# Performance work log

Measured on AMD Instinct MI355X. Metric: run time of the kernel, lower is better.

Reference implementation:

```python
import jax, jax.numpy as jnp
import numpy as np

EPS = 1e-5


def conv1x1(x, w, b=None):
    # x: [B,C,H,W], w: [O,C] (1x1 conv kernel squeezed)
    y = jnp.einsum('bchw,oc->bohw', x, w)
    if b is not None:
        y = y + b[None, :, None, None]
    return y


def bn_inf(x, g, b, m, v):
    scale = g / jnp.sqrt(v + EPS)
    return (x - m[None, :, None, None]) * scale[None, :, None, None] + b[None, :, None, None]


def setup_inputs() -> dict:
    B, C, H, W = 2, 256, 80, 80
    Ck, Cv, Co = 64, 128, 256
    key = jax.random.key(0)
    ks = jax.random.split(key, 16)
    d = {}
    d['x'] = jax.random.normal(ks[0], (B, C, H, W), dtype=jnp.float32)
    d['y'] = jax.random.normal(ks[1], (B, C, H, W), dtype=jnp.float32)
    s = 1.0 / np.sqrt(C)
    d['fk_w'] = jax.random.normal(ks[2], (Ck, C), dtype=jnp.float32) * s
    d['fk_g'] = jnp.ones((Ck,), jnp.float32)
    d['fk_b'] = jnp.zeros((Ck,), jnp.float32)
    d['fk_m'] = jax.random.normal(ks[3], (Ck,), dtype=jnp.float32) * 0.1
    d['fk_v'] = jax.random.uniform(ks[4], (Ck,), minval=0.5, maxval=1.5, dtype=jnp.float32)
    d['fq_w'] = jax.random.normal(ks[5], (Ck, C), dtype=jnp.float32) * s
    d['fq_g'] = jnp.ones((Ck,), jnp.float32)
    d['fq_b'] = jnp.zeros((Ck,), jnp.float32)
    d['fq_m'] = jax.random.normal(ks[6], (Ck,), dtype=jnp.float32) * 0.1
    d['fq_v'] = jax.random.uniform(ks[7], (Ck,), minval=0.5, maxval=1.5, dtype=jnp.float32)
    d['fv_w'] = jax.random.normal(ks[8], (Cv, C), dtype=jnp.float32) * s
    d['fv_b'] = jnp.zeros((Cv,), jnp.float32)
    d['W_w'] = jax.random.normal(ks[9], (Co, Cv), dtype=jnp.float32) * (1.0 / np.sqrt(Cv))
    d['W_b'] = jnp.zeros((Co,), jnp.float32)
    d['gamma'] = jnp.array([0.5], jnp.float32)
    return d


def reference(x, y, fk_w, fk_g, fk_b, fk_m, fk_v, fq_w, fq_g, fq_b, fq_m, fq_v, fv_w, fv_b, W_w, W_b, gamma):
    B, C, H, W = x.shape
    Ck = fk_w.shape[0]
    Cv = fv_w.shape[0]
    N = H * W
    # key from x, query/value from y (1x1 conv + BN projections)
    k = bn_inf(conv1x1(x, fk_w), fk_g, fk_b, fk_m, fk_v).reshape(B, Ck, N)          # [B,Ck,N]
    q = bn_inf(conv1x1(y, fq_w), fq_g, fq_b, fq_m, fq_v).reshape(B, Ck, N)          # [B,Ck,N]
    v = conv1x1(y, fv_w, fv_b).reshape(B, Cv, N)                                     # [B,Cv,N]
    sim = jnp.einsum('bkn,bkm->bnm', q, k) * (Ck ** -0.5)                            # [B,N,N]
    sim = jax.nn.softmax(sim, axis=-1)
    ctx = jnp.einsum('bnm,bvm->bvn', sim, v).reshape(B, Cv, H, W)                    # [B,Cv,H,W]
    ctx = conv1x1(ctx, W_w, W_b)                                                     # [B,Co,H,W]
    return gamma[0] * ctx + x
```

## Files before the change

### kernel.cpp

```cpp
#include <hip/hip_runtime.h>
#include <math.h>

#define NB   2
#define CIN  256
#define NN   6400
#define CKd  64
#define CVd  128
#define COd  256

using bf16   = __bf16;
using bf16x4 = __attribute__((ext_vector_type(4))) bf16;
using bf16x8 = __attribute__((ext_vector_type(8))) bf16;
using f32x4  = __attribute__((ext_vector_type(4))) float;

__device__ __forceinline__ void lds_cp16(const void* g, void* l) {
    __builtin_amdgcn_global_load_lds((const __attribute__((address_space(1))) void*)g,
                                     (__attribute__((address_space(3))) void*)l, 16, 0, 0);
}

__global__ void prep_kernel(const float* __restrict__ fk_w, const float* __restrict__ fk_g,
                            const float* __restrict__ fk_b, const float* __restrict__ fk_m,
                            const float* __restrict__ fk_v,
                            const float* __restrict__ fq_w, const float* __restrict__ fq_g,
                            const float* __restrict__ fq_b, const float* __restrict__ fq_m,
                            const float* __restrict__ fq_v,
                            const float* __restrict__ fv_w, const float* __restrict__ fv_b,
                            const float* __restrict__ W_w,  const float* __restrict__ W_b,
                            bf16* __restrict__ wkb, bf16* __restrict__ wqb,
                            bf16* __restrict__ wvb, bf16* __restrict__ wob,
                            float* __restrict__ bias)
{
    const int idx = blockIdx.x * 256 + threadIdx.x;
    if (idx < 16384) {
        const int co = idx >> 8;
        const float a = fk_g[co] * rsqrtf(fk_v[co] + 1e-5f);
        wkb[idx] = (bf16)(fk_w[idx] * a);
    } else if (idx < 32768) {
        const int i = idx - 16384, co = i >> 8;
        const float a = fq_g[co] * rsqrtf(fq_v[co] + 1e-5f) * 0.125f;
        wqb[i] = (bf16)(fq_w[i] * a);
    } else if (idx < 65536) {
        const int i = idx - 32768;
        wvb[i] = (bf16)fv_w[i];
    } else if (idx < 98304) {
        const int i = idx - 65536;
        wob[i] = (bf16)W_w[i];
    } else if (idx < 98816) {
        const int j = idx - 98304;
        if (j < 64)       { const float a = fk_g[j] * rsqrtf(fk_v[j] + 1e-5f); bias[j] = fk_b[j] - fk_m[j] * a; }
        else if (j < 128) { const int c = j - 64; const float a = fq_g[c] * rsqrtf(fq_v[c] + 1e-5f); bias[j] = (fq_b[c] - fq_m[c] * a) * 0.125f; }
        else if (j < 256) bias[j] = fv_b[j - 128];
        else              bias[j] = W_b[j - 256];
    }
}

__launch_bounds__(256)
__global__ void tcvt_kernel(const float* __restrict__ x, const float* __restrict__ y,
                            bf16* __restrict__ xT, bf16* __restrict__ yT)
{
    __shared__ __align__(16) bf16 t_lds[64][68];
    const int b = blockIdx.z & 1;
    const float* src = (blockIdx.z >> 1) ? y : x;
    bf16* dst = (blockIdx.z >> 1) ? yT : xT;
    const int n0 = blockIdx.x * 64, c0 = blockIdx.y * 64;
    const int tid = threadIdx.x;
    const int nl = (tid & 15) * 4;
#pragma unroll
    for (int p = 0; p < 4; ++p) {
        const int cl = (tid >> 4) + p * 16;
        const float4 v = *(const float4*)(src + (size_t)(b * CIN + c0 + cl) * NN + n0 + nl);
        t_lds[nl + 0][cl] = (bf16)v.x;
        t_lds[nl + 1][cl] = (bf16)v.y;
        t_lds[nl + 2][cl] = (bf16)v.z;
        t_lds[nl + 3][cl] = (bf16)v.w;
    }
    __syncthreads();
#pragma unroll
    for (int p = 0; p < 4; ++p) {
        const int u = tid + p * 256;
        const int n = u >> 4, c4 = (u & 15) * 4;
        const bf16x4 pk = *(const bf16x4*)&t_lds[n][c4];
        *(bf16x4*)(dst + ((size_t)b * NN + n0 + n) * CIN + c0 + c4) = pk;
    }
}

__launch_bounds__(256, 2)
__global__ void projkqv_kernel(const bf16* __restrict__ xT, const bf16* __restrict__ yT,
                               const bf16* __restrict__ wkb, const bf16* __restrict__ wqb,
                               const bf16* __restrict__ wvb, const float* __restrict__ bias,
                               bf16* __restrict__ kb, bf16* __restrict__ qb, bf16* __restrict__ vb)
{
    __shared__ __align__(16) bf16 sbuf[64 * 256];
    __shared__ __align__(16) bf16 wbuf[64 * 256];

    const int tid  = threadIdx.x;
    const int lane = tid & 63, wav = tid >> 6;
    const int l15  = lane & 15, quad = lane >> 4;
    const int b    = blockIdx.z, m = blockIdx.y;
    const int n0   = blockIdx.x * 64;

    const bf16* srcg = ((m == 0) ? xT : yT) + ((size_t)b * NN + n0) * CIN;
    const bf16* wg   = (m == 0) ? wkb : (m == 1) ? wqb : (wvb + (size_t)(m - 2) * 64 * CIN);

    const int r2  = lane >> 5;
    const int c32 = lane & 31;
#pragma unroll
    for (int i = 0; i < 8; ++i) {
        const int rg = wav * 16 + i * 2;
        const int r  = rg + r2;
        const int cs = c32 ^ (r & 7);
        lds_cp16(srcg + (size_t)r * 256 + cs * 8, &sbuf[rg * 256]);
        lds_cp16(wg   + (size_t)r * 256 + cs * 8, &wbuf[rg * 256]);
    }
    __syncthreads();

    const int key = l15 & 7;
    f32x4 acc[4];
#pragma unroll
    for (int j = 0; j < 4; ++j) acc[j] = (f32x4){0.f, 0.f, 0.f, 0.f};

    if (m < 2) {
        const int arow = wav * 16 + l15;
#pragma unroll
        for (int k4 = 0; k4 < 32; k4 += 4) {
            const bf16x8 af = *(const bf16x8*)&sbuf[arow * 256 + ((k4 + quad) ^ key) * 8];
#pragma unroll
            for (int nt = 0; nt < 4; ++nt) {
                const int brow = nt * 16 + l15;
                const bf16x8 bfw = *(const bf16x8*)&wbuf[brow * 256 + ((k4 + quad) ^ key) * 8];
                acc[nt] = __builtin_amdgcn_mfma_f32_16x16x32_bf16(af, bfw, acc[nt], 0, 0, 0);
            }
        }
        const float* bs = bias + m * 64;
        bf16* dst = (m == 0) ? kb : qb;
        const int nb = n0 + wav * 16;
#pragma unroll
        for (int nt = 0; nt < 4; ++nt) {
            const float bv = bs[nt * 16 + l15];
#pragma unroll
            for (int r = 0; r < 4; ++r) {
                const int n = nb + quad * 4 + r;
                dst[((size_t)b * NN + n) * CKd + nt * 16 + l15] = (bf16)(acc[nt][r] + bv);
            }
        }
    } else {
        const int arow = wav * 16 + l15;
#pragma unroll
        for (int k4 = 0; k4 < 32; k4 += 4) {
            const bf16x8 af = *(const bf16x8*)&wbuf[arow * 256 + ((k4 + quad) ^ key) * 8];
#pragma unroll
            for (int nt = 0; nt < 4; ++nt) {
                const int brow = nt * 16 + l15;
                const bf16x8 bfy = *(const bf16x8*)&sbuf[brow * 256 + ((k4 + quad) ^ key) * 8];
                acc[nt] = __builtin_amdgcn_mfma_f32_16x16x32_bf16(af, bfy, acc[nt], 0, 0, 0);
            }
        }
        const int cv0 = (m - 2) * 64 + wav * 16;
#pragma unroll
        for (int r = 0; r < 4; ++r) {
            const int cv = cv0 + quad * 4 + r;
            const float bv = bias[128 + cv];
#pragma unroll
            for (int nt = 0; nt < 4; ++nt)
                vb[((size_t)b * CVd + cv) * NN + n0 + nt * 16 + l15] = (bf16)(acc[nt][r] + bv);
        }
    }
}

__launch_bounds__(256, 3)
__global__ void attn_kernel(const bf16* __restrict__ qb, const bf16* __restrict__ kb,
                            const bf16* __restrict__ vb,
                            bf16* __restrict__ pO, float* __restrict__ pl,
                            int tpc, int kmask, int kbits)
{
    __shared__ __align__(16) bf16 kbuf[2][64 * 64];
    __shared__ __align__(16) bf16 vbuf[2][128 * 64];
    __shared__ __align__(16) bf16 p_lds[4][2][16][64];

    const int lane = threadIdx.x & 63;
    const int wav  = threadIdx.x >> 6;
    const int l15  = lane & 15;
    const int quad = lane >> 4;
    const int r8   = lane >> 3;
    const int c_src = (lane & 7) ^ r8;
    const int sw   = l15 & 7;
    const int pkey = (l15 & 7) << 1;

    const int id    = blockIdx.x;
    const int ks    = id & kmask;
    const int b     = (id >> kbits) & 1;
    const int qtile = id >> (kbits + 1);
    const int q0    = qtile * 128 + wav * 32;

    const bf16* qrow = qb + (size_t)b * NN * CKd;
    const bf16* krow = kb + (size_t)b * NN * CKd;
    const bf16* vrow = vb + (size_t)b * CVd * NN;

    bf16x8 qf[2][2];
#pragma unroll
    for (int qt = 0; qt < 2; ++qt)
#pragma unroll
        for (int s = 0; s < 2; ++s)
            qf[qt][s] = *(const bf16x8*)(qrow + (size_t)(q0 + qt * 16 + l15) * CKd + s * 32 + quad * 8);

    f32x4 acc[2][8];
#pragma unroll
    for (int qt = 0; qt < 2; ++qt)
#pragma unroll
        for (int cv = 0; cv < 8; ++cv) acc[qt][cv] = (f32x4){0.f, 0.f, 0.f, 0.f};
    float psum[2] = {0.f, 0.f};

    const int t0  = ks * tpc;
    const int rem = 100 - t0;
    const int nt  = (tpc < rem) ? tpc : rem;

    auto stage = [&](int t, int bi) {
        const int key0 = t * 64;
        lds_cp16(krow + (size_t)(key0 + wav * 8 + r8) * CKd + c_src * 8,
                 &kbuf[bi][(wav * 8) * 64]);
        lds_cp16(krow + (size_t)(key0 + (wav + 4) * 8 + r8) * CKd + c_src * 8,
                 &kbuf[bi][((wav + 4) * 8) * 64]);
#pragma unroll
        for (int g4 = 0; g4 < 4; ++g4) {
            const int g = wav * 4 + g4;
            lds_cp16(vrow + (size_t)(g * 8 + r8) * NN + key0 + c_src * 8,
                     &vbuf[bi][(g * 8) * 64]);
        }
    };

    stage(t0, 0);

    for (int t = 0; t < nt; ++t) {
        __syncthreads();
        if (t + 1 < nt) stage(t0 + t + 1, (t + 1) & 1);
        const bf16* kcur = &kbuf[t & 1][0];
        const bf16* vcur = &vbuf[t & 1][0];

        f32x4 s4[2][4];
#pragma unroll
        for (int kt = 0; kt < 4; ++kt) {
            const int rr = kt * 16 + l15;
            const bf16x8 kf0 = *(const bf16x8*)&kcur[rr * 64 + ((quad ^ sw) * 8)];
            const bf16x8 kf1 = *(const bf16x8*)&kcur[rr * 64 + (((4 + quad) ^ sw) * 8)];
#pragma unroll
            for (int qt = 0; qt < 2; ++qt) {
                f32x4 z = (f32x4){0.f, 0.f, 0.f, 0.f};
                z = __builtin_amdgcn_mfma_f32_16x16x32_bf16(kf0, qf[qt][0], z, 0, 0, 0);
                z = __builtin_amdgcn_mfma_f32_16x16x32_bf16(kf1, qf[qt][1], z, 0, 0, 0);
                s4[qt][kt] = z;
            }
        }

#pragma unroll
        for (int qt = 0; qt < 2; ++qt) {
            float ps = 0.f;
#pragma unroll
            for (int kt = 0; kt < 4; ++kt) {
                bf16x4 pk;
#pragma unroll
                for (int r = 0; r < 4; ++r) {
                    const float p = exp2f(fmaf(s4[qt][kt][r], 1.4426950408889634f, -11.541560327111707f));
                    ps += p;
                    pk[r] = (bf16)p;
                }
                *(bf16x4*)&p_lds[wav][qt][l15][((kt * 4 + quad) ^ pkey) * 4] = pk;
            }
            psum[qt] += ps;
        }

        bf16x8 pf[2][2];
#pragma unroll
        for (int qt = 0; qt < 2; ++qt)
#pragma unroll
            for (int sp = 0; sp < 2; ++sp)
                pf[qt][sp] = *(const bf16x8*)&p_lds[wav][qt][l15][((sp * 8 + quad * 2) ^ pkey) * 4];

#pragma unroll
        for (int sp = 0; sp < 2; ++sp)
#pragma unroll
            for (int cvt = 0; cvt < 8; ++cvt) {
                const int rr = cvt * 16 + l15;
                const bf16x8 vf = *(const bf16x8*)&vcur[rr * 64 + (((sp * 4 + quad) ^ sw) * 8)];
                acc[0][cvt] = __builtin_amdgcn_mfma_f32_16x16x32_bf16(vf, pf[0][sp], acc[0][cvt], 0, 0, 0);
                acc[1][cvt] = __builtin_amdgcn_mfma_f32_16x16x32_bf16(vf, pf[1][sp], acc[1][cvt], 0, 0, 0);
            }
    }

    __syncthreads();
    bf16* tbuf = &p_lds[wav][0][0][0];
    const size_t pb = (size_t)ks * NB + b;
#pragma unroll
    for (int qt = 0; qt < 2; ++qt) {
        psum[qt] += __shfl_xor(psum[qt], 16);
        psum[qt] += __shfl_xor(psum[qt], 32);
#pragma unroll
        for (int cvt = 0; cvt < 8; ++cvt) {
            bf16x4 pk;
#pragma unroll
            for (int r = 0; r < 4; ++r) pk[r] = (bf16)acc[qt][cvt][r];
            const int u = (cvt * 4 + quad) ^ ((l15 & 15) << 1);
            *(bf16x4*)&tbuf[l15 * 128 + u * 4] = pk;
        }
#pragma unroll
        for (int j = 0; j < 4; ++j) {
            const int row = j * 4 + (lane >> 4);
            const int g   = ((lane & 15) * 2) ^ ((row & 15) << 1);
            const bf16x8 vv = *(const bf16x8*)&tbuf[row * 128 + g * 4];
            *(bf16x8*)(pO + (pb * NN + q0 + qt * 16) * CVd + j * 512 + lane * 8) = vv;
        }
        if (quad == 0) pl[pb * NN + q0 + qt * 16 + l15] = psum[qt];
    }
}

__launch_bounds__(256, 2)
__global__ void outproj_kernel(const bf16* __restrict__ pO, const float* __restrict__ pl,
                               const bf16* __restrict__ wob, const float* __restrict__ bias,
                               const float* __restrict__ x, const float* __restrict__ gam,
                               float* __restrict__ out, int KS)
{
    __shared__ __align__(16) bf16 wbuf[256 * 128];
    __shared__ __align__(16) bf16 cbuf[32 * 128];
    __shared__ float Lrow[32];

    const int tid  = threadIdx.x;
    const int lane = tid & 63, wav = tid >> 6;
    const int l15  = lane & 15, quad = lane >> 4;
    const int b    = blockIdx.y;
    const int n0   = blockIdx.x * 32;

    {
        const int r4 = lane >> 4;
        const int c  = lane & 15;
#pragma unroll
        for (int i = 0; i < 16; ++i) {
            const int rg = wav * 64 + i * 4;
            const int r  = rg + r4;
            const int cs = c ^ (r & 7);
            lds_cp16(wob + (size_t)r * CVd + cs * 8, &wbuf[rg * 128]);
        }
    }

    const int tn = tid >> 3;
    const int tc = (tid & 7) * 16;
    float vacc[16];
#pragma unroll
    for (int i = 0; i < 16; ++i) vacc[i] = 0.f;
    for (int ksi = 0; ksi < KS; ++ksi) {
        const bf16* src = pO + ((size_t)(ksi * NB + b) * NN + n0 + tn) * CVd + tc;
#pragma unroll
        for (int j = 0; j < 2; ++j) {
            const bf16x8 v = *(const bf16x8*)(src + j * 8);
#pragma unroll
            for (int e = 0; e < 8; ++e) vacc[j * 8 + e] += (float)v[e];
        }
    }
    if (tid < 32) {
        float L = 0.f;
        for (int ksi = 0; ksi < KS; ++ksi)
            L += pl[(size_t)(ksi * NB + b) * NN + n0 + tid];
        Lrow[tid] = 1.0f / L;
    }
    __syncthreads();
    {
        const float rL = Lrow[tn];
#pragma unroll
        for (int j = 0; j < 2; ++j) {
            bf16x8 o;
#pragma unroll
            for (int e = 0; e < 8; ++e) o[e] = (bf16)(vacc[j * 8 + e] * rL);
            const int c = (tid & 7) * 2 + j;
            *(bf16x8*)&cbuf[tn * 128 + ((c ^ (tn & 7)) * 8)] = o;
        }
    }
    __syncthreads();

    f32x4 acc[4][2];
#pragma unroll
    for (int i = 0; i < 4; ++i)
#pragma unroll
        for (int j = 0; j < 2; ++j) acc[i][j] = (f32x4){0.f, 0.f, 0.f, 0.f};

#pragma unroll
    for (int kk = 0; kk < 4; ++kk) {
#pragma unroll
        for (int cot = 0; cot < 4; ++cot) {
            const int arow = wav * 64 + cot * 16 + l15;
            const bf16x8 af = *(const bf16x8*)&wbuf[arow * 128 + (((kk * 4 + quad) ^ (arow & 7)) * 8)];
#pragma unroll
            for (int nt = 0; nt < 2; ++nt) {
                const int brow = nt * 16 + l15;
                const bf16x8 bfc = *(const bf16x8*)&cbuf[brow * 128 + (((kk * 4 + quad) ^ (brow & 7)) * 8)];
                acc[cot][nt] = __builtin_amdgcn_mfma_f32_16x16x32_bf16(af, bfc, acc[cot][nt], 0, 0, 0);
            }
        }
    }

    const float gm = gam[0];
#pragma unroll
    for (int cot = 0; cot < 4; ++cot) {
#pragma unroll
        for (int r = 0; r < 4; ++r) {
            const int co = wav * 64 + cot * 16 + quad * 4 + r;
            const float bv = bias[256 + co];
#pragma unroll
            for (int nt = 0; nt < 2; ++nt) {
                const int n = n0 + nt * 16 + l15;
                const size_t a = ((size_t)b * COd + co) * NN + n;
                out[a] = gm * (acc[cot][nt][r] + bv) + x[a];
            }
        }
    }
}

extern "C" void kernel_launch(void* const* d_in, const int* in_sizes, int n_in,
                              void* d_out, int out_size, void* d_ws, size_t ws_size,
                              hipStream_t stream)
{
    const float* x     = (const float*)d_in[0];
    const float* y     = (const float*)d_in[1];
    const float* fk_w  = (const float*)d_in[2];
    const float* fk_g  = (const float*)d_in[3];
    const float* fk_b  = (const float*)d_in[4];
    const float* fk_m  = (const float*)d_in[5];
    const float* fk_v  = (const float*)d_in[6];
    const float* fq_w  = (const float*)d_in[7];
    const float* fq_g  = (const float*)d_in[8];
    const float* fq_b  = (const float*)d_in[9];
    const float* fq_m  = (const float*)d_in[10];
    const float* fq_v  = (const float*)d_in[11];
    const float* fv_w  = (const float*)d_in[12];
    const float* fv_b  = (const float*)d_in[13];
    const float* W_w   = (const float*)d_in[14];
    const float* W_b   = (const float*)d_in[15];
    const float* gamma = (const float*)d_in[16];
    float* out = (float*)d_out;

    char* ws = (char*)d_ws;
    size_t off = 0;
    auto carve = [&](size_t bytes) -> char* {
        char* p = ws + off;
        off = (off + bytes + 255) & ~(size_t)255;
        return p;
    };

    bf16*  kb   = (bf16*)carve((size_t)NB * NN * CKd * 2);
    bf16*  qbuf = (bf16*)carve((size_t)NB * NN * CKd * 2);
    bf16*  vb   = (bf16*)carve((size_t)NB * CVd * NN * 2);
    bf16*  wkb  = (bf16*)carve((size_t)CKd * CIN * 2);
    bf16*  wqb  = (bf16*)carve((size_t)CKd * CIN * 2);
    bf16*  wvb  = (bf16*)carve((size_t)CVd * CIN * 2);
    bf16*  wob  = (bf16*)carve((size_t)COd * CVd * 2);
    float* bias = (float*)carve(512 * 4);

    const size_t alias_start = off;
    bf16* xT = (bf16*)carve((size_t)NB * NN * CIN * 2);
    bf16* yT = (bf16*)carve((size_t)NB * NN * CIN * 2);

    const size_t region = ws_size - alias_start;
    const size_t per_ks = (size_t)NB * NN * CVd * 2 + (size_t)NB * NN * 4 + 512;
    int KS = 1, kbits = 0;
    {
        const int cand[4] = {8, 4, 2, 1};
        const int cbit[4] = {3, 2, 1, 0};
        for (int i = 0; i < 4; ++i)
            if ((size_t)cand[i] * per_ks <= region) { KS = cand[i]; kbits = cbit[i]; break; }
    }
    bf16*  pO = (bf16*)(ws + alias_start);
    float* pl = (float*)(ws + alias_start + (size_t)KS * NB * NN * CVd * 2);
    const int tpc = (100 + KS - 1) / KS;

    const dim3 blk(256);
    prep_kernel<<<386, blk, 0, stream>>>(fk_w, fk_g, fk_b, fk_m, fk_v,
                                         fq_w, fq_g, fq_b, fq_m, fq_v,
                                         fv_w, fv_b, W_w, W_b,
                                         wkb, wqb, wvb, wob, bias);
    tcvt_kernel<<<dim3(100, 4, 4), blk, 0, stream>>>(x, y, xT, yT);
    projkqv_kernel<<<dim3(100, 4, NB), blk, 0, stream>>>(xT, yT, wkb, wqb, wvb, bias, kb, qbuf, vb);
    attn_kernel<<<dim3(50 * NB * KS), blk, 0, stream>>>(qbuf, kb, vb, pO, pl, tpc, KS - 1, kbits);
    outproj_kernel<<<dim3(200, NB), blk, 0, stream>>>(pO, pl, wob, bias, x, gamma, out, KS);
}
```

Baseline: 189.9 us.

## Enlarge attention query tile per wave and fuse weight prep into transpose kernel

Each attention wave now handles 64 queries instead of 32, in two phases, so every K/V tile staged in LDS is reused across twice as many queries. The key-split factor can now be non-power-of-two (up to 10) to keep enough blocks in flight, and the grid is halved per split. The 1/sqrt(Ck) scale is folded together with log2(e) into the query weights, which removes an FMA in the softmax exponent. The separate weight-prep launch is merged into the transpose/convert kernel as an extra grid slice, saving one launch. The cost is more accumulator registers, so occupancy drops from 3 to 2 blocks per CU, and it adds integer division and modulo for the block index mapping.

```diff
diff --git a/kernel.cpp b/kernel.cpp
--- a/kernel.cpp
+++ b/kernel.cpp
@@ -18,47 +18,50 @@
                                      (__attribute__((address_space(3))) void*)l, 16, 0, 0);
 }
 
-__global__ void prep_kernel(const float* __restrict__ fk_w, const float* __restrict__ fk_g,
-                            const float* __restrict__ fk_b, const float* __restrict__ fk_m,
-                            const float* __restrict__ fk_v,
-                            const float* __restrict__ fq_w, const float* __restrict__ fq_g,
-                            const float* __restrict__ fq_b, const float* __restrict__ fq_m,
-                            const float* __restrict__ fq_v,
-                            const float* __restrict__ fv_w, const float* __restrict__ fv_b,
-                            const float* __restrict__ W_w,  const float* __restrict__ W_b,
-                            bf16* __restrict__ wkb, bf16* __restrict__ wqb,
-                            bf16* __restrict__ wvb, bf16* __restrict__ wob,
-                            float* __restrict__ bias)
-{
-    const int idx = blockIdx.x * 256 + threadIdx.x;
-    if (idx < 16384) {
-        const int co = idx >> 8;
-        const float a = fk_g[co] * rsqrtf(fk_v[co] + 1e-5f);
-        wkb[idx] = (bf16)(fk_w[idx] * a);
-    } else if (idx < 32768) {
-        const int i = idx - 16384, co = i >> 8;
-        const float a = fq_g[co] * rsqrtf(fq_v[co] + 1e-5f) * 0.125f;
-        wqb[i] = (bf16)(fq_w[i] * a);
-    } else if (idx < 65536) {
-        const int i = idx - 32768;
-        wvb[i] = (bf16)fv_w[i];
-    } else if (idx < 98304) {
-        const int i = idx - 65536;
-        wob[i] = (bf16)W_w[i];
-    } else if (idx < 98816) {
-        const int j = idx - 98304;
-        if (j < 64)       { const float a = fk_g[j] * rsqrtf(fk_v[j] + 1e-5f); bias[j] = fk_b[j] - fk_m[j] * a; }
-        else if (j < 128) { const int c = j - 64; const float a = fq_g[c] * rsqrtf(fq_v[c] + 1e-5f); bias[j] = (fq_b[c] - fq_m[c] * a) * 0.125f; }
-        else if (j < 256) bias[j] = fv_b[j - 128];
-        else              bias[j] = W_b[j - 256];
-    }
-}
-
 __launch_bounds__(256)
-__global__ void tcvt_kernel(const float* __restrict__ x, const float* __restrict__ y,
-                            bf16* __restrict__ xT, bf16* __restrict__ yT)
+__global__ void tcvt_prep_kernel(const float* __restrict__ x, const float* __restrict__ y,
+                                 bf16* __restrict__ xT, bf16* __restrict__ yT,
+                                 const float* __restrict__ fk_w, const float* __restrict__ fk_g,
+                                 const float* __restrict__ fk_b, const float* __restrict__ fk_m,
+                                 const float* __restrict__ fk_v,
+                                 const float* __restrict__ fq_w, const float* __restrict__ fq_g,
+                                 const float* __restrict__ fq_b, const float* __restrict__ fq_m,
+                                 const float* __restrict__ fq_v,
+                                 const float* __restrict__ fv_w, const float* __restrict__ fv_b,
+                                 const float* __restrict__ W_w,  const float* __restrict__ W_b,
+                                 bf16* __restrict__ wkb, bf16* __restrict__ wqb,
+                                 bf16* __restrict__ wvb, bf16* __restrict__ wob,
+                                 float* __restrict__ bias)
 {
     __shared__ __align__(16) bf16 t_lds[64][68];
+
+    if (blockIdx.z == 4) {
+        const int idx = (blockIdx.y * 100 + blockIdx.x) * 256 + threadIdx.x;
+        const float QS = 0.18033688011112042f;
+        if (idx < 16384) {
+            const int co = idx >> 8;
+            const float a = fk_g[co] * rsqrtf(fk_v[co] + 1e-5f);
+            wkb[idx] = (bf16)(fk_w[idx] * a);
+        } else if (idx < 32768) {
+            const int i = idx - 16384, co = i >> 8;
+            const float a = fq_g[co] * rsqrtf(fq_v[co] + 1e-5f) * QS;
+            wqb[i] = (bf16)(fq_w[i] * a);
+        } else if (idx < 65536) {
+            const int i = idx - 32768;
+            wvb[i] = (bf16)fv_w[i];
+        } else if (idx < 98304) {
+            const int i = idx - 65536;
+            wob[i] = (bf16)W_w[i];
+        } else if (idx < 98816) {
+            const int j = idx - 98304;
+            if (j < 64)       { const float a = fk_g[j] * rsqrtf(fk_v[j] + 1e-5f); bias[j] = fk_b[j] - fk_m[j] * a; }
+            else if (j < 128) { const int c = j - 64; const float a = fq_g[c] * rsqrtf(fq_v[c] + 1e-5f); bias[j] = (fq_b[c] - fq_m[c] * a) * QS; }
+            else if (j < 256) bias[j] = fv_b[j - 128];
+            else              bias[j] = W_b[j - 256];
+        }
+        return;
+    }
+
     const int b = blockIdx.z & 1;
     const float* src = (blockIdx.z >> 1) ? y : x;
     bf16* dst = (blockIdx.z >> 1) ? yT : xT;
@@ -167,11 +170,10 @@
     }
 }
 
-__launch_bounds__(256, 3)
+__launch_bounds__(256, 2)
 __global__ void attn_kernel(const bf16* __restrict__ qb, const bf16* __restrict__ kb,
                             const bf16* __restrict__ vb,
-                            bf16* __restrict__ pO, float* __restrict__ pl,
-                            int tpc, int kmask, int kbits)
+                            bf16* __restrict__ pO, float* __restrict__ pl, int KS)
 {
     __shared__ __align__(16) bf16 kbuf[2][64 * 64];
     __shared__ __align__(16) bf16 vbuf[2][128 * 64];
@@ -187,32 +189,32 @@
     const int pkey = (l15 & 7) << 1;
 
     const int id    = blockIdx.x;
-    const int ks    = id & kmask;
-    const int b     = (id >> kbits) & 1;
-    const int qtile = id >> (kbits + 1);
-    const int q0    = qtile * 128 + wav * 32;
+    const int ks    = id % KS;
+    const int rst   = id / KS;
+    const int b     = rst & 1;
+    const int qtile = rst >> 1;
+    const int q0    = qtile * 256 + wav * 64;
 
     const bf16* qrow = qb + (size_t)b * NN * CKd;
     const bf16* krow = kb + (size_t)b * NN * CKd;
     const bf16* vrow = vb + (size_t)b * CVd * NN;
 
-    bf16x8 qf[2][2];
-#pragma unroll
-    for (int qt = 0; qt < 2; ++qt)
+    bf16x8 qf[4][2];
+#pragma unroll
+    for (int qt = 0; qt < 4; ++qt)
 #pragma unroll
         for (int s = 0; s < 2; ++s)
             qf[qt][s] = *(const bf16x8*)(qrow + (size_t)(q0 + qt * 16 + l15) * CKd + s * 32 + quad * 8);
 
-    f32x4 acc[2][8];
-#pragma unroll
-    for (int qt = 0; qt < 2; ++qt)
+    f32x4 acc[4][8];
+#pragma unroll
+    for (int qt = 0; qt < 4; ++qt)
 #pragma unroll
         for (int cv = 0; cv < 8; ++cv) acc[qt][cv] = (f32x4){0.f, 0.f, 0.f, 0.f};
-    float psum[2] = {0.f, 0.f};
-
-    const int t0  = ks * tpc;
-    const int rem = 100 - t0;
-    const int nt  = (tpc < rem) ? tpc : rem;
+    float psum[4] = {0.f, 0.f, 0.f, 0.f};
+
+    const int t0 = (100 * ks) / KS;
+    const int nt = (100 * (ks + 1)) / KS - t0;
 
     auto stage = [&](int t, int bi) {
         const int key0 = t * 64;
@@ -236,61 +238,61 @@
         const bf16* kcur = &kbuf[t & 1][0];
         const bf16* vcur = &vbuf[t & 1][0];
 
-        f32x4 s4[2][4];
-#pragma unroll
-        for (int kt = 0; kt < 4; ++kt) {
-            const int rr = kt * 16 + l15;
-            const bf16x8 kf0 = *(const bf16x8*)&kcur[rr * 64 + ((quad ^ sw) * 8)];
-            const bf16x8 kf1 = *(const bf16x8*)&kcur[rr * 64 + (((4 + quad) ^ sw) * 8)];
-#pragma unroll
-            for (int qt = 0; qt < 2; ++qt) {
-                f32x4 z = (f32x4){0.f, 0.f, 0.f, 0.f};
-                z = __builtin_amdgcn_mfma_f32_16x16x32_bf16(kf0, qf[qt][0], z, 0, 0, 0);
-                z = __builtin_amdgcn_mfma_f32_16x16x32_bf16(kf1, qf[qt][1], z, 0, 0, 0);
-                s4[qt][kt] = z;
-            }
-        }
-
-#pragma unroll
-        for (int qt = 0; qt < 2; ++qt) {
-            float ps = 0.f;
+#pragma unroll
+        for (int ph = 0; ph < 2; ++ph) {
+            f32x4 s4[2][4];
 #pragma unroll
             for (int kt = 0; kt < 4; ++kt) {
-                bf16x4 pk;
-#pragma unroll
-                for (int r = 0; r < 4; ++r) {
-                    const float p = exp2f(fmaf(s4[qt][kt][r], 1.4426950408889634f, -11.541560327111707f));
-                    ps += p;
-                    pk[r] = (bf16)p;
+                const int rr = kt * 16 + l15;
+                const bf16x8 kf0 = *(const bf16x8*)&kcur[rr * 64 + ((quad ^ sw) * 8)];
+                const bf16x8 kf1 = *(const bf16x8*)&kcur[rr * 64 + (((4 + quad) ^ sw) * 8)];
+#pragma unroll
+                for (int qtl = 0; qtl < 2; ++qtl) {
+                    const int qt = ph * 2 + qtl;
+                    f32x4 z = (f32x4){0.f, 0.f, 0.f, 0.f};
+                    z = __builtin_amdgcn_mfma_f32_16x16x32_bf16(kf0, qf[qt][0], z, 0, 0, 0);
+                    z = __builtin_amdgcn_mfma_f32_16x16x32_bf16(kf1, qf[qt][1], z, 0, 0, 0);
+                    s4[qtl][kt] = z;
                 }
-                *(bf16x4*)&p_lds[wav][qt][l15][((kt * 4 + quad) ^ pkey) * 4] = pk;
-            }
-            psum[qt] += ps;
-        }
-
-        bf16x8 pf[2][2];
-#pragma unroll
-        for (int qt = 0; qt < 2; ++qt)
-#pragma unroll
-            for (int sp = 0; sp < 2; ++sp)
-                pf[qt][sp] = *(const bf16x8*)&p_lds[wav][qt][l15][((sp * 8 + quad * 2) ^ pkey) * 4];
-
-#pragma unroll
-        for (int sp = 0; sp < 2; ++sp)
-#pragma unroll
-            for (int cvt = 0; cvt < 8; ++cvt) {
-                const int rr = cvt * 16 + l15;
-                const bf16x8 vf = *(const bf16x8*)&vcur[rr * 64 + (((sp * 4 + quad) ^ sw) * 8)];
-                acc[0][cvt] = __builtin_amdgcn_mfma_f32_16x16x32_bf16(vf, pf[0][sp], acc[0][cvt], 0, 0, 0);
-                acc[1][cvt] = __builtin_amdgcn_mfma_f32_16x16x32_bf16(vf, pf[1][sp], acc[1][cvt], 0, 0, 0);
-            }
+            }
+
+#pragma unroll
+            for (int qtl = 0; qtl < 2; ++qtl) {
+                float ps = 0.f;
+#pragma unroll
+                for (int kt = 0; kt < 4; ++kt) {
+                    bf16x4 pk;
+#pragma unroll
+                    for (int r = 0; r < 4; ++r) {
+                        const float p = exp2f(s4[qtl][kt][r] - 11.541560327111707f);
+                        ps += p;
+                        pk[r] = (bf16)p;
+                    }
+                    *(bf16x4*)&p_lds[wav][qtl][l15][((kt * 4 + quad) ^ pkey) * 4] = pk;
+                }
+                psum[ph * 2 + qtl] += ps;
+            }
+
+#pragma unroll
+            for (int sp = 0; sp < 2; ++sp) {
+                const bf16x8 pf0 = *(const bf16x8*)&p_lds[wav][0][l15][((sp * 8 + quad * 2) ^ pkey) * 4];
+                const bf16x8 pf1 = *(const bf16x8*)&p_lds[wav][1][l15][((sp * 8 + quad * 2) ^ pkey) * 4];
+#pragma unroll
+                for (int cvt = 0; cvt < 8; ++cvt) {
+                    const int rr = cvt * 16 + l15;
+                    const bf16x8 vf = *(const bf16x8*)&vcur[rr * 64 + (((sp * 4 + quad) ^ sw) * 8)];
+                    acc[ph * 2 + 0][cvt] = __builtin_amdgcn_mfma_f32_16x16x32_bf16(vf, pf0, acc[ph * 2 + 0][cvt], 0, 0, 0);
+                    acc[ph * 2 + 1][cvt] = __builtin_amdgcn_mfma_f32_16x16x32_bf16(vf, pf1, acc[ph * 2 + 1][cvt], 0, 0, 0);
+                }
+            }
+        }
     }
 
     __syncthreads();
     bf16* tbuf = &p_lds[wav][0][0][0];
     const size_t pb = (size_t)ks * NB + b;
 #pragma unroll
-    for (int qt = 0; qt < 2; ++qt) {
+    for (int qt = 0; qt < 4; ++qt) {
         psum[qt] += __shfl_xor(psum[qt], 16);
         psum[qt] += __shfl_xor(psum[qt], 32);
 #pragma unroll
@@ -298,7 +300,7 @@
             bf16x4 pk;
 #pragma unroll
             for (int r = 0; r < 4; ++r) pk[r] = (bf16)acc[qt][cvt][r];
-            const int u = (cvt * 4 + quad) ^ ((l15 & 15) << 1);
+            const int u = (cvt * 4 + quad) ^ (l15 << 1);
             *(bf16x4*)&tbuf[l15 * 128 + u * 4] = pk;
         }
 #pragma unroll
@@ -458,24 +460,22 @@
 
     const size_t region = ws_size - alias_start;
     const size_t per_ks = (size_t)NB * NN * CVd * 2 + (size_t)NB * NN * 4 + 512;
-    int KS = 1, kbits = 0;
+    int KS = 1;
     {
-        const int cand[4] = {8, 4, 2, 1};
-        const int cbit[4] = {3, 2, 1, 0};
-        for (int i = 0; i < 4; ++i)
-            if ((size_t)cand[i] * per_ks <= region) { KS = cand[i]; kbits = cbit[i]; break; }
+        const int cand[6] = {10, 8, 5, 4, 2, 1};
+        for (int i = 0; i < 6; ++i)
+            if ((size_t)cand[i] * per_ks <= region) { KS = cand[i]; break; }
     }
     bf16*  pO = (bf16*)(ws + alias_start);
     float* pl = (float*)(ws + alias_start + (size_t)KS * NB * NN * CVd * 2);
-    const int tpc = (100 + KS - 1) / KS;
 
     const dim3 blk(256);
-    prep_kernel<<<386, blk, 0, stream>>>(fk_w, fk_g, fk_b, fk_m, fk_v,
-                                         fq_w, fq_g, fq_b, fq_m, fq_v,
-                                         fv_w, fv_b, W_w, W_b,
-                                         wkb, wqb, wvb, wob, bias);
-    tcvt_kernel<<<dim3(100, 4, 4), blk, 0, stream>>>(x, y, xT, yT);
+    tcvt_prep_kernel<<<dim3(100, 4, 5), blk, 0, stream>>>(x, y, xT, yT,
+                                                          fk_w, fk_g, fk_b, fk_m, fk_v,
+                                                          fq_w, fq_g, fq_b, fq_m, fq_v,
+                                                          fv_w, fv_b, W_w, W_b,
+                                                          wkb, wqb, wvb, wob, bias);
     projkqv_kernel<<<dim3(100, 4, NB), blk, 0, stream>>>(xT, yT, wkb, wqb, wvb, bias, kb, qbuf, vb);
-    attn_kernel<<<dim3(50 * NB * KS), blk, 0, stream>>>(qbuf, kb, vb, pO, pl, tpc, KS - 1, kbits);
+    attn_kernel<<<dim3(25 * NB * KS), blk, 0, stream>>>(qbuf, kb, vb, pO, pl, KS);
     outproj_kernel<<<dim3(200, NB), blk, 0, stream>>>(pO, pl, wob, bias, x, gamma, out, KS);
 }
```

Measured after the change: 174.4 us. -8.2%, faster.
